# Kernel tuning notes

Hardware: AMD Instinct MI355X
Metric: run time of the kernel (lower is better)

Reference implementation:

```python
import jax, jax.numpy as jnp
import numpy as np

N_NODES = 100000
N_EDGES = 1600000
N_REL = 8
N_HEADS = 4
IN_FEAT = 128
OUT_FEAT = 64
D_HEAD = OUT_FEAT // N_HEADS
LEAKY_SLOPE = 0.2


def setup_inputs() -> dict:
    key = jax.random.key(0)
    ks = jax.random.split(key, 8)
    inputs = jax.random.normal(ks[0], (N_NODES, IN_FEAT), dtype=jnp.float32)
    conv_weights = jax.random.normal(ks[1], (N_REL, N_HEADS, IN_FEAT, D_HEAD), dtype=jnp.float32) * (1.0 / np.sqrt(IN_FEAT))
    attn_l = jax.random.normal(ks[2], (N_REL, N_HEADS, D_HEAD), dtype=jnp.float32) * (1.0 / np.sqrt(D_HEAD))
    attn_r = jax.random.normal(ks[3], (N_REL, N_HEADS, D_HEAD), dtype=jnp.float32) * (1.0 / np.sqrt(D_HEAD))
    h_bias = jax.random.normal(ks[4], (OUT_FEAT,), dtype=jnp.float32)
    src_idx = jax.random.randint(ks[5], (N_EDGES,), 0, N_NODES, dtype=jnp.int64) if jax.config.jax_enable_x64 else jax.random.randint(ks[5], (N_EDGES,), 0, N_NODES, dtype=jnp.int32)
    dst_idx = jax.random.randint(ks[6], (N_EDGES,), 0, N_NODES, dtype=src_idx.dtype)
    rel_idx = jax.random.randint(ks[7], (N_EDGES,), 0, N_REL, dtype=src_idx.dtype)
    return {"inputs": inputs, "conv_weights": conv_weights, "attn_l": attn_l,
            "attn_r": attn_r, "h_bias": h_bias, "src_idx": src_idx,
            "dst_idx": dst_idx, "rel_idx": rel_idx}


def reference(inputs, conv_weights, attn_l, attn_r, h_bias, src_idx, dst_idx, rel_idx):
    N = inputs.shape[0]
    # Per-node per-relation projection: [N, R, H, Dh]
    # (equivalent math to the per-relation grouped matmul over unique nodes)
    proj = jnp.einsum('ni,rhid->nrhd', inputs, conv_weights)
    # Gather per-edge src/dst projected features under the edge's relation: [E, H, Dh]
    feat_src = proj[src_idx, rel_idx]
    feat_dst = proj[dst_idx, rel_idx]
    # Attention logits per edge/head: [E, H]
    el = jnp.sum(feat_src * attn_l[rel_idx], axis=-1)
    er = jnp.sum(feat_dst * attn_r[rel_idx], axis=-1)
    score = jax.nn.leaky_relu(el + er, negative_slope=LEAKY_SLOPE)
    # Edge softmax over incoming edges of each destination node (per head)
    smax = jax.ops.segment_max(score, dst_idx, num_segments=N)        # [N, H]
    e = jnp.exp(score - smax[dst_idx])                                # [E, H]
    denom = jax.ops.segment_sum(e, dst_idx, num_segments=N)          # [N, H]
    alpha = e / denom[dst_idx]                                        # [E, H]
    # Weighted aggregation of src features to dst nodes: [N, H, Dh]
    h = jax.ops.segment_sum(alpha[..., None] * feat_src, dst_idx, num_segments=N)
    h = h.reshape(N, OUT_FEAT) + h_bias
    return h
```

## Files before the change

### kernel.cpp

```cpp
#include <hip/hip_runtime.h>
#include <hip/hip_bf16.h>


#define NN 100000
#define NNP 100096
#define NE 1600000
#define NH 4
#define INF_ 128
#define DH 16
#define NCOL 576
#define LEAKY 0.2f
#define NBUCK 391
#define BSHIFT 8
#define CHUNK 4096
#define CAP 5120
#define GEMM_BLOCKS 782
#define WEXT_BLOCKS 288

typedef __hip_bfloat16 bf16;
typedef __attribute__((ext_vector_type(8))) short bf16x8;
typedef __attribute__((ext_vector_type(4))) short bf16x4;
typedef __attribute__((ext_vector_type(4))) float f32x4;

static __device__ __forceinline__ short f2bs(float x) {
    bf16 b = __float2bfloat16(x);
    return *reinterpret_cast<short*>(&b);
}
static __device__ __forceinline__ float bflo(unsigned u) { return __uint_as_float(u << 16); }
static __device__ __forceinline__ float bfhi(unsigned u) { return __uint_as_float(u & 0xffff0000u); }
static __device__ __forceinline__ float b2f(short us) {
    return __uint_as_float(((unsigned)(unsigned short)us) << 16);
}

__global__ void build_wextT(const float* __restrict__ W, const float* __restrict__ al,
                            const float* __restrict__ ar, short* __restrict__ wxt2,
                            int* __restrict__ gCursor) {
    if (blockIdx.x >= WEXT_BLOCKS) {
        int i = (blockIdx.x - WEXT_BLOCKS) * 256 + threadIdx.x;
        if (i < NBUCK) gCursor[i] = 0;
        return;
    }
    int idx = blockIdx.x * 256 + threadIdx.x;
    int e = idx & 7, lane = (idx >> 3) & 63, ct = (idx >> 9) & 3, ks = (idx >> 11) & 3, cb = idx >> 13;
    int g = lane >> 4, r = lane & 15;
    int c = cb * 64 + ct * 16 + r;
    int k = ks * 32 + g * 8 + e;
    float v;
    if (c < 512) {
        int rr = c >> 6, rem = c & 63, h = rem >> 4, d = rem & 15;
        v = W[((rr * NH + h) * INF_ + k) * DH + d];
    } else {
        int rh = c - 512;
        const float* a = al;
        if (rh >= 32) { rh -= 32; a = ar; }
        int rr = rh >> 2, h = rh & 3;
        const float* wp = &W[((rr * NH + h) * INF_ + k) * DH];
        const float* ap = &a[(rr * NH + h) * DH];
        float s = 0.f;
        #pragma unroll
        for (int d = 0; d < DH; ++d) s += wp[d] * ap[d];
        v = s;
    }
    wxt2[idx] = f2bs(v);
}

__global__ __launch_bounds__(256) void gemm_fused(
    const float* __restrict__ A, const short* __restrict__ WxT2,
    short* __restrict__ projR, short* __restrict__ elrb,
    const int* __restrict__ src, const int* __restrict__ dst, const int* __restrict__ rel,
    int* __restrict__ gCursor, int* __restrict__ pairbuf) {
    __shared__ short As[16384];
    int t = threadIdx.x;

    if (blockIdx.x >= GEMM_BLOCKS) {
        int* hist = (int*)As;
        int blk = blockIdx.x - GEMM_BLOCKS;
        for (int i = t; i < NBUCK; i += 256) hist[i] = 0;
        __syncthreads();
        int base = blk * CHUNK;
        #pragma unroll
        for (int j = 0; j < CHUNK / 256; ++j) {
            int e = base + j * 256 + t;
            if (e < NE) atomicAdd(&hist[dst[e] >> BSHIFT], 1);
        }
        __syncthreads();
        for (int i = t; i < NBUCK; i += 256) {
            int v = hist[i];
            hist[i] = v ? (i * CAP + atomicAdd(&gCursor[i], v)) : 0;
        }
        __syncthreads();
        #pragma unroll
        for (int j = 0; j < CHUNK / 256; ++j) {
            int e = base + j * 256 + t;
            if (e < NE) {
                int d = dst[e];
                int b = d >> BSHIFT;
                int rec = ((d & 255) << 20) | (src[e] * 8 + rel[e]);
                int pos = atomicAdd(&hist[b], 1);
                pairbuf[pos] = rec;
            }
        }
        return;
    }

    int wv = t >> 6, lane = t & 63;
    int n0 = blockIdx.x * 128;
    int g = lane >> 4, r = lane & 15;

    #pragma unroll
    for (int j = 0; j < 8; ++j) {
        int i = j * 256 + t;
        int row = i >> 4, c8 = i & 15;
        int gr = n0 + row;
        bf16x8 v;
        if (gr < NN) {
            float4 f0 = *(const float4*)&A[gr * INF_ + c8 * 8];
            float4 f1 = *(const float4*)&A[gr * INF_ + c8 * 8 + 4];
            v[0] = f2bs(f0.x); v[1] = f2bs(f0.y); v[2] = f2bs(f0.z); v[3] = f2bs(f0.w);
            v[4] = f2bs(f1.x); v[5] = f2bs(f1.y); v[6] = f2bs(f1.z); v[7] = f2bs(f1.w);
        } else {
            v = (bf16x8)(short)0;
        }
        *(bf16x8*)&As[(row * 16 + (c8 ^ (row & 7))) * 8] = v;
    }
    __syncthreads();

    bf16x8 afr[2][4];
    #pragma unroll
    for (int nt = 0; nt < 2; ++nt) {
        int row = wv * 32 + nt * 16 + r;
        #pragma unroll
        for (int ks = 0; ks < 4; ++ks)
            afr[nt][ks] = *(const bf16x8*)&As[(row * 16 + ((ks * 4 + g) ^ (r & 7))) * 8];
    }
    __syncthreads();
    short* Csh = &As[wv * 4096];
    int n0w = n0 + wv * 32;

    for (int cb = 0; cb < 9; ++cb) {
        f32x4 acc[2][4] = {};
        #pragma unroll
        for (int ks = 0; ks < 4; ++ks) {
            #pragma unroll
            for (int ct = 0; ct < 4; ++ct) {
                bf16x8 b = *(const bf16x8*)&WxT2[(((cb * 4 + ks) * 4 + ct) * 64 + lane) * 8];
                acc[0][ct] = __builtin_amdgcn_mfma_f32_16x16x32_bf16(b, afr[0][ks], acc[0][ct], 0, 0, 0);
                acc[1][ct] = __builtin_amdgcn_mfma_f32_16x16x32_bf16(b, afr[1][ks], acc[1][ct], 0, 0, 0);
            }
        }
        #pragma unroll
        for (int nt = 0; nt < 2; ++nt) {
            int rr = nt * 16 + r;
            #pragma unroll
            for (int ct = 0; ct < 4; ++ct) {
                bf16x4 p;
                p[0] = f2bs(acc[nt][ct][0]); p[1] = f2bs(acc[nt][ct][1]);
                p[2] = f2bs(acc[nt][ct][2]); p[3] = f2bs(acc[nt][ct][3]);
                *(bf16x4*)&Csh[rr * 64 + (((ct * 4 + g) ^ ((rr & 7) << 1)) << 2)] = p;
            }
        }
        __builtin_amdgcn_wave_barrier();
        short* dstbase = (cb < 8) ? &projR[((size_t)cb * NN + n0w) * 64]
                                  : &elrb[(size_t)n0w * 64];
        #pragma unroll
        for (int q = 0; q < 4; ++q) {
            int rr = (lane >> 3) + q * 8;
            if (n0w + rr < NN) {
                bf16x8 vv = *(const bf16x8*)&Csh[rr * 64 + (((lane & 7) ^ (rr & 7)) << 3)];
                *(bf16x8*)&dstbase[q * 512 + lane * 8] = vv;
            }
        }
        __builtin_amdgcn_wave_barrier();
    }
}

__global__ __launch_bounds__(256) void exact_place(
    const int* __restrict__ gCursor, const int* __restrict__ pairbuf,
    int2* __restrict__ offdeg, int* __restrict__ rec) {
    __shared__ int hist[256];
    __shared__ int tsum[256];
    int b = blockIdx.x, t = threadIdx.x;
    int start = b * CAP, cnt = gCursor[b];
    hist[t] = 0;
    __syncthreads();
    for (int i = t; i < cnt; i += 256) atomicAdd(&hist[pairbuf[start + i] >> 20], 1);
    __syncthreads();
    int own = hist[t];
    tsum[t] = own;
    __syncthreads();
    for (int st = 1; st < 256; st <<= 1) {
        int y = (t >= st) ? tsum[t - st] : 0;
        __syncthreads();
        tsum[t] += y;
        __syncthreads();
    }
    int excl = start + tsum[t] - own;
    int node = b * 256 + t;
    if (node < NN) offdeg[node] = make_int2(excl, own);
    __syncthreads();
    hist[t] = excl;
    __syncthreads();
    for (int i = t; i < cnt; i += 256) {
        int rc = pairbuf[start + i];
        int pos = atomicAdd(&hist[rc >> 20], 1);
        int sr = rc & 0xFFFFF;
        rec[pos] = (sr >> 3) * 64 + (sr & 7) * 4;
    }
}

__global__ __launch_bounds__(256) void agg(
    const int2* __restrict__ offdeg, const int* __restrict__ rec,
    const short* __restrict__ elrb, const bf16* __restrict__ projR,
    const float* __restrict__ bias, float* __restrict__ out) {
    __shared__ float s_alpha[4][64][4];
    __shared__ int   s_pidx[4][64];
    __shared__ float s_er[4][32];
    int wv = threadIdx.x >> 6, lane = threadIdx.x & 63;
    int d = blockIdx.x * 4 + wv;
    if (d >= NN) return;
    int2 od = offdeg[d];
    int off = od.x, deg = od.y;
    int end = off + deg;

    if (lane < 32) s_er[wv][lane] = b2f(elrb[d * 64 + 32 + lane]);
    __builtin_amdgcn_wave_barrier();
    asm volatile("s_waitcnt lgkmcnt(0)" ::: "memory");

    if (deg == 0) {
        if (lane < 32) {
            float2 bb = *(const float2*)&bias[lane * 2];
            *(float2*)&out[d * 64 + lane * 2] = bb;
        }
    } else if (deg <= 64) {
        int i = off + lane;
        float e0 = 0.f, e1 = 0.f, e2 = 0.f, e3 = 0.f;
        int pidx = 0;
        if (i < end) {
            int rv = rec[i];
            pidx = ((rv & 63) >> 2) * (NN * 64) + (rv >> 6) * 64;
            bf16x4 el4 = *(const bf16x4*)&elrb[rv];
            int erb = rv & 63;
            float x;
            x = b2f(el4[0]) + s_er[wv][erb + 0]; x = x > 0.f ? x : LEAKY * x; e0 = __expf(x);
            x = b2f(el4[1]) + s_er[wv][erb + 1]; x = x > 0.f ? x : LEAKY * x; e1 = __expf(x);
            x = b2f(el4[2]) + s_er[wv][erb + 2]; x = x > 0.f ? x : LEAKY * x; e2 = __expf(x);
            x = b2f(el4[3]) + s_er[wv][erb + 3]; x = x > 0.f ? x : LEAKY * x; e3 = __expf(x);
        }
        s_pidx[wv][lane] = pidx;
        *(float4*)&s_alpha[wv][lane][0] = make_float4(e0, e1, e2, e3);
        __builtin_amdgcn_wave_barrier();
        asm volatile("s_waitcnt lgkmcnt(0)" ::: "memory");

        int col2 = (lane & 31) * 2;
        int hl = lane >> 5;
        int h2 = (lane & 31) >> 3;
        float acc0 = 0.f, acc1 = 0.f, dsum = 0.f;
        int j = 0;
        for (; j + 8 <= deg; j += 8) {
            unsigned uu[4];
            #pragma unroll
            for (int p = 0; p < 4; ++p) {
                int myp = s_pidx[wv][j + 2 * p + hl];
                uu[p] = *(const unsigned*)&projR[myp + col2];
            }
            #pragma unroll
            for (int p = 0; p < 4; ++p) {
                float a_self = s_alpha[wv][j + 2 * p + hl][h2];
                float a_oth  = s_alpha[wv][j + 2 * p + 1 - hl][h2];
                unsigned uo = __shfl_xor((int)uu[p], 32);
                acc0 = fmaf(a_self, bflo(uu[p]), acc0);
                acc1 = fmaf(a_self, bfhi(uu[p]), acc1);
                acc0 = fmaf(a_oth, bflo(uo), acc0);
                acc1 = fmaf(a_oth, bfhi(uo), acc1);
                dsum += a_self + a_oth;
            }
        }
        for (; j + 2 <= deg; j += 2) {
            int myp = s_pidx[wv][j + hl];
            unsigned u = *(const unsigned*)&projR[myp + col2];
            float a_self = s_alpha[wv][j + hl][h2];
            float a_oth  = s_alpha[wv][j + 1 - hl][h2];
            unsigned uo = __shfl_xor((int)u, 32);
            acc0 = fmaf(a_self, bflo(u), acc0);
            acc1 = fmaf(a_self, bfhi(u), acc1);
            acc0 = fmaf(a_oth, bflo(uo), acc0);
            acc1 = fmaf(a_oth, bfhi(uo), acc1);
            dsum += a_self + a_oth;
        }
        if (j < deg) {
            int myp = s_pidx[wv][j];
            unsigned u = *(const unsigned*)&projR[myp + col2];
            float a = s_alpha[wv][j][h2];
            acc0 = fmaf(a, bflo(u), acc0);
            acc1 = fmaf(a, bfhi(u), acc1);
            dsum += a;
        }
        if (lane < 32) {
            float inv = 1.0f / dsum;
            float2 bb = *(const float2*)&bias[col2];
            float2 o;
            o.x = acc0 * inv + bb.x;
            o.y = acc1 * inv + bb.y;
            *(float2*)&out[d * 64 + col2] = o;
        }
    } else {
        int c = lane, h = c >> 4;
        float dsum0 = 0.f, dsum1 = 0.f, dsum2 = 0.f, dsum3 = 0.f;
        for (int i = off + lane; i < end; i += 64) {
            int rv = rec[i];
            bf16x4 el4 = *(const bf16x4*)&elrb[rv];
            int erb = rv & 63;
            float x;
            x = b2f(el4[0]) + s_er[wv][erb + 0]; x = x > 0.f ? x : LEAKY * x; dsum0 += __expf(x);
            x = b2f(el4[1]) + s_er[wv][erb + 1]; x = x > 0.f ? x : LEAKY * x; dsum1 += __expf(x);
            x = b2f(el4[2]) + s_er[wv][erb + 2]; x = x > 0.f ? x : LEAKY * x; dsum2 += __expf(x);
            x = b2f(el4[3]) + s_er[wv][erb + 3]; x = x > 0.f ? x : LEAKY * x; dsum3 += __expf(x);
        }
        #pragma unroll
        for (int m = 32; m; m >>= 1) {
            dsum0 += __shfl_xor(dsum0, m, 64);
            dsum1 += __shfl_xor(dsum1, m, 64);
            dsum2 += __shfl_xor(dsum2, m, 64);
            dsum3 += __shfl_xor(dsum3, m, 64);
        }
        float dh = (h == 0) ? dsum0 : (h == 1) ? dsum1 : (h == 2) ? dsum2 : dsum3;
        float rd = 1.0f / dh;
        float acc = 0.f;
        for (int i = off; i < end; ++i) {
            int rv = rec[i];
            int pidx = ((rv & 63) >> 2) * (NN * 64) + (rv >> 6) * 64;
            float x = b2f(elrb[rv + h]) + s_er[wv][(rv & 63) + h];
            x = x > 0.f ? x : LEAKY * x;
            acc = fmaf(__expf(x) * rd, __bfloat162float(projR[pidx + c]), acc);
        }
        out[d * 64 + c] = acc + bias[c];
    }
}

extern "C" void kernel_launch(void* const* d_in, const int* in_sizes, int n_in,
                              void* d_out, int out_size, void* d_ws, size_t ws_size,
                              hipStream_t stream) {
    const float* inputs = (const float*)d_in[0];
    const float* convw  = (const float*)d_in[1];
    const float* attn_l = (const float*)d_in[2];
    const float* attn_r = (const float*)d_in[3];
    const float* h_bias = (const float*)d_in[4];
    const int*   src    = (const int*)d_in[5];
    const int*   dst    = (const int*)d_in[6];
    const int*   rel    = (const int*)d_in[7];
    float* out = (float*)d_out;

    char* ws = (char*)d_ws;
    size_t o = 0;
    bf16* projR  = (bf16*)(ws + o);  o += 102400000ull;
    short* elrb  = (short*)(ws + o); o += 12800000ull;
    short* wxt2  = (short*)(ws + o); o += 147456;
    int2* offdeg = (int2*)(ws + o);  o += 800768;
    int* gCursor = (int*)(ws + o);   o += 2048;
    int* pairbuf = (int*)(ws + o);   o += (size_t)NBUCK * CAP * 4;
    int* rec     = (int*)(ws + o);   o += (size_t)NBUCK * CAP * 4;

    hipLaunchKernelGGL(build_wextT, dim3(WEXT_BLOCKS + 2), dim3(256), 0, stream,
                       convw, attn_l, attn_r, wxt2, gCursor);
    hipLaunchKernelGGL(gemm_fused, dim3(GEMM_BLOCKS + NBUCK), dim3(256), 0, stream,
                       inputs, wxt2, (short*)projR, elrb, src, dst, rel, gCursor, pairbuf);
    hipLaunchKernelGGL(exact_place, dim3(NBUCK), dim3(256), 0, stream, gCursor, pairbuf, offdeg, rec);
    hipLaunchKernelGGL(agg, dim3(25000), dim3(256), 0, stream, offdeg, rec, elrb, projR, h_bias, out);
}
```

Before: 138.8 us.

## Rebalance kernel stages and stage GEMM weights through shared memory with prefetch

Moves the edge bucket scatter into the weight-building kernel and the exact per-node placement into the GEMM kernel. This drops one launch and lets the placement work overlap with the GEMM blocks. The gCursor reset becomes a memset. The GEMM now loads each 64-column weight block into shared memory once per block, prefetching the next block into registers, instead of every wave reading weights from global memory. This adds block-wide barriers per column block and extra LDS use, which may lower occupancy.

```diff
diff --git a/kernel.cpp b/kernel.cpp
--- a/kernel.cpp
+++ b/kernel.cpp
@@ -32,15 +32,45 @@
     return __uint_as_float(((unsigned)(unsigned short)us) << 16);
 }
 
-__global__ void build_wextT(const float* __restrict__ W, const float* __restrict__ al,
-                            const float* __restrict__ ar, short* __restrict__ wxt2,
-                            int* __restrict__ gCursor) {
+__global__ __launch_bounds__(256) void wext_scatter(
+    const float* __restrict__ W, const float* __restrict__ al, const float* __restrict__ ar,
+    short* __restrict__ wxt2,
+    const int* __restrict__ src, const int* __restrict__ dst, const int* __restrict__ rel,
+    int* __restrict__ gCursor, int* __restrict__ pairbuf) {
+    __shared__ int hist[NBUCK];
+    int t = threadIdx.x;
+
     if (blockIdx.x >= WEXT_BLOCKS) {
-        int i = (blockIdx.x - WEXT_BLOCKS) * 256 + threadIdx.x;
-        if (i < NBUCK) gCursor[i] = 0;
+        int blk = blockIdx.x - WEXT_BLOCKS;
+        for (int i = t; i < NBUCK; i += 256) hist[i] = 0;
+        __syncthreads();
+        int base = blk * CHUNK;
+        #pragma unroll
+        for (int j = 0; j < CHUNK / 256; ++j) {
+            int e = base + j * 256 + t;
+            if (e < NE) atomicAdd(&hist[dst[e] >> BSHIFT], 1);
+        }
+        __syncthreads();
+        for (int i = t; i < NBUCK; i += 256) {
+            int v = hist[i];
+            hist[i] = v ? (i * CAP + atomicAdd(&gCursor[i], v)) : 0;
+        }
+        __syncthreads();
+        #pragma unroll
+        for (int j = 0; j < CHUNK / 256; ++j) {
+            int e = base + j * 256 + t;
+            if (e < NE) {
+                int d = dst[e];
+                int b = d >> BSHIFT;
+                int rec = ((d & 255) << 20) | (src[e] * 8 + rel[e]);
+                int pos = atomicAdd(&hist[b], 1);
+                pairbuf[pos] = rec;
+            }
+        }
         return;
     }
-    int idx = blockIdx.x * 256 + threadIdx.x;
+
+    int idx = blockIdx.x * 256 + t;
     int e = idx & 7, lane = (idx >> 3) & 63, ct = (idx >> 9) & 3, ks = (idx >> 11) & 3, cb = idx >> 13;
     int g = lane >> 4, r = lane & 15;
     int c = cb * 64 + ct * 16 + r;
@@ -64,41 +94,44 @@
     wxt2[idx] = f2bs(v);
 }
 
-__global__ __launch_bounds__(256) void gemm_fused(
+__global__ __launch_bounds__(256) void gemm_place(
     const float* __restrict__ A, const short* __restrict__ WxT2,
     short* __restrict__ projR, short* __restrict__ elrb,
-    const int* __restrict__ src, const int* __restrict__ dst, const int* __restrict__ rel,
-    int* __restrict__ gCursor, int* __restrict__ pairbuf) {
+    const int* __restrict__ gCursor, const int* __restrict__ pairbuf,
+    int2* __restrict__ offdeg, int* __restrict__ rec) {
     __shared__ short As[16384];
+    __shared__ short Bs[8192];
     int t = threadIdx.x;
 
     if (blockIdx.x >= GEMM_BLOCKS) {
         int* hist = (int*)As;
-        int blk = blockIdx.x - GEMM_BLOCKS;
-        for (int i = t; i < NBUCK; i += 256) hist[i] = 0;
-        __syncthreads();
-        int base = blk * CHUNK;
-        #pragma unroll
-        for (int j = 0; j < CHUNK / 256; ++j) {
-            int e = base + j * 256 + t;
-            if (e < NE) atomicAdd(&hist[dst[e] >> BSHIFT], 1);
-        }
-        __syncthreads();
-        for (int i = t; i < NBUCK; i += 256) {
-            int v = hist[i];
-            hist[i] = v ? (i * CAP + atomicAdd(&gCursor[i], v)) : 0;
-        }
-        __syncthreads();
-        #pragma unroll
-        for (int j = 0; j < CHUNK / 256; ++j) {
-            int e = base + j * 256 + t;
-            if (e < NE) {
-                int d = dst[e];
-                int b = d >> BSHIFT;
-                int rec = ((d & 255) << 20) | (src[e] * 8 + rel[e]);
-                int pos = atomicAdd(&hist[b], 1);
-                pairbuf[pos] = rec;
-            }
+        int* tsum = hist + 256;
+        int b = blockIdx.x - GEMM_BLOCKS;
+        int start = b * CAP, cnt = gCursor[b];
+        hist[t] = 0;
+        __syncthreads();
+        for (int i = t; i < cnt; i += 256) atomicAdd(&hist[pairbuf[start + i] >> 20], 1);
+        __syncthreads();
+        int own = hist[t];
+        tsum[t] = own;
+        __syncthreads();
+        for (int st = 1; st < 256; st <<= 1) {
+            int y = (t >= st) ? tsum[t - st] : 0;
+            __syncthreads();
+            tsum[t] += y;
+            __syncthreads();
+        }
+        int excl = start + tsum[t] - own;
+        int node = b * 256 + t;
+        if (node < NN) offdeg[node] = make_int2(excl, own);
+        __syncthreads();
+        hist[t] = excl;
+        __syncthreads();
+        for (int i = t; i < cnt; i += 256) {
+            int rc = pairbuf[start + i];
+            int pos = atomicAdd(&hist[rc >> 20], 1);
+            int sr = rc & 0xFFFFF;
+            rec[pos] = (sr >> 3) * 64 + (sr & 7) * 4;
         }
         return;
     }
@@ -123,6 +156,10 @@
         }
         *(bf16x8*)&As[(row * 16 + (c8 ^ (row & 7))) * 8] = v;
     }
+    bf16x8 breg[4];
+    #pragma unroll
+    for (int q = 0; q < 4; ++q)
+        breg[q] = *(const bf16x8*)&WxT2[(q * 256 + t) * 8];
     __syncthreads();
 
     bf16x8 afr[2][4];
@@ -138,12 +175,22 @@
     int n0w = n0 + wv * 32;
 
     for (int cb = 0; cb < 9; ++cb) {
+        #pragma unroll
+        for (int q = 0; q < 4; ++q)
+            *(bf16x8*)&Bs[(q * 256 + t) * 8] = breg[q];
+        __syncthreads();
+        if (cb < 8) {
+            #pragma unroll
+            for (int q = 0; q < 4; ++q)
+                breg[q] = *(const bf16x8*)&WxT2[((cb + 1) * 1024 + q * 256 + t) * 8];
+        }
+
         f32x4 acc[2][4] = {};
         #pragma unroll
         for (int ks = 0; ks < 4; ++ks) {
             #pragma unroll
             for (int ct = 0; ct < 4; ++ct) {
-                bf16x8 b = *(const bf16x8*)&WxT2[(((cb * 4 + ks) * 4 + ct) * 64 + lane) * 8];
+                bf16x8 b = *(const bf16x8*)&Bs[((ks * 4 + ct) * 64 + lane) * 8];
                 acc[0][ct] = __builtin_amdgcn_mfma_f32_16x16x32_bf16(b, afr[0][ks], acc[0][ct], 0, 0, 0);
                 acc[1][ct] = __builtin_amdgcn_mfma_f32_16x16x32_bf16(b, afr[1][ks], acc[1][ct], 0, 0, 0);
             }
@@ -170,41 +217,7 @@
                 *(bf16x8*)&dstbase[q * 512 + lane * 8] = vv;
             }
         }
-        __builtin_amdgcn_wave_barrier();
-    }
-}
-
-__global__ __launch_bounds__(256) void exact_place(
-    const int* __restrict__ gCursor, const int* __restrict__ pairbuf,
-    int2* __restrict__ offdeg, int* __restrict__ rec) {
-    __shared__ int hist[256];
-    __shared__ int tsum[256];
-    int b = blockIdx.x, t = threadIdx.x;
-    int start = b * CAP, cnt = gCursor[b];
-    hist[t] = 0;
-    __syncthreads();
-    for (int i = t; i < cnt; i += 256) atomicAdd(&hist[pairbuf[start + i] >> 20], 1);
-    __syncthreads();
-    int own = hist[t];
-    tsum[t] = own;
-    __syncthreads();
-    for (int st = 1; st < 256; st <<= 1) {
-        int y = (t >= st) ? tsum[t - st] : 0;
-        __syncthreads();
-        tsum[t] += y;
-        __syncthreads();
-    }
-    int excl = start + tsum[t] - own;
-    int node = b * 256 + t;
-    if (node < NN) offdeg[node] = make_int2(excl, own);
-    __syncthreads();
-    hist[t] = excl;
-    __syncthreads();
-    for (int i = t; i < cnt; i += 256) {
-        int rc = pairbuf[start + i];
-        int pos = atomicAdd(&hist[rc >> 20], 1);
-        int sr = rc & 0xFFFFF;
-        rec[pos] = (sr >> 3) * 64 + (sr & 7) * 4;
+        __syncthreads();
     }
 }
 
@@ -360,10 +373,10 @@
     int* pairbuf = (int*)(ws + o);   o += (size_t)NBUCK * CAP * 4;
     int* rec     = (int*)(ws + o);   o += (size_t)NBUCK * CAP * 4;
 
-    hipLaunchKernelGGL(build_wextT, dim3(WEXT_BLOCKS + 2), dim3(256), 0, stream,
-                       convw, attn_l, attn_r, wxt2, gCursor);
-    hipLaunchKernelGGL(gemm_fused, dim3(GEMM_BLOCKS + NBUCK), dim3(256), 0, stream,
-                       inputs, wxt2, (short*)projR, elrb, src, dst, rel, gCursor, pairbuf);
-    hipLaunchKernelGGL(exact_place, dim3(NBUCK), dim3(256), 0, stream, gCursor, pairbuf, offdeg, rec);
+    hipMemsetAsync(gCursor, 0, NBUCK * sizeof(int), stream);
+    hipLaunchKernelGGL(wext_scatter, dim3(WEXT_BLOCKS + NBUCK), dim3(256), 0, stream,
+                       convw, attn_l, attn_r, wxt2, src, dst, rel, gCursor, pairbuf);
+    hipLaunchKernelGGL(gemm_place, dim3(GEMM_BLOCKS + NBUCK), dim3(256), 0, stream,
+                       inputs, wxt2, (short*)projR, elrb, gCursor, pairbuf, offdeg, rec);
     hipLaunchKernelGGL(agg, dim3(25000), dim3(256), 0, stream, offdeg, rec, elrb, projR, h_bias, out);
 }
```

After: 135.3 us. 1.03x faster.
